# Performance work log

Hardware: AMD Instinct MI355X
Metric: run time of the kernel (lower is better)

Reference implementation:

```python
import jax, jax.numpy as jnp
import numpy as np

B, N_IN, N_OUT = 4096, 64, 64
M = N_IN * N_OUT


def setup_inputs() -> dict:
    key = jax.random.key(0)
    k1, k2, k3, k4 = jax.random.split(key, 4)
    I = jax.random.normal(k1, (B, N_IN, 4, 4), dtype=jnp.float32)
    # params: (rand - 0.5) * 1, matching torch init
    aW = (jax.random.uniform(k2, (M, 1, 1), dtype=jnp.float32) - 0.5)
    uW = (jax.random.uniform(k3, (M, 1, 3), dtype=jnp.float32) - 0.5)
    tW = (jax.random.uniform(k4, (M, 1, 3), dtype=jnp.float32) - 0.5)
    return {"I": I, "aW": aW, "uW": uW, "tW": tW}


def _build_WM(aW, uW, tW, n_in, n_out):
    m = aW.shape[0]
    a = aW.reshape(m, 1, 1)                       # angle per transform
    u = jax.nn.sigmoid(uW.reshape(m, 3))
    u = u / jnp.linalg.norm(u, axis=1, keepdims=True)  # unit axis
    ux, uy, uz = u[:, 0], u[:, 1], u[:, 2]
    z = jnp.zeros_like(ux)
    # skew-symmetric cross-product matrix K
    K = jnp.stack([z, -uz, uy,
                   uz, z, -ux,
                   -uy, ux, z], axis=1).reshape(m, 3, 3)
    uuT = u[:, :, None] * u[:, None, :]
    I3 = jnp.eye(3, dtype=aW.dtype)
    # Rodrigues: R = sin(a) K + cos(a)(I - uu^T) + uu^T
    rot = jnp.sin(a) * K + jnp.cos(a) * (I3 - uuT) + uuT
    top = jnp.concatenate([rot, tW.reshape(m, 3, 1)], axis=2)   # [m,3,4]
    bot = jnp.broadcast_to(jnp.array([[0.0, 0.0, 0.0, 1.0]], dtype=aW.dtype), (m, 1, 4))
    WM = jnp.concatenate([top, bot], axis=1)                    # [m,4,4]
    return WM.reshape(n_in, n_out, 4, 4)


def reference(I, aW, uW, tW):
    batch, n_in = I.shape[0], I.shape[1]
    n_out = aW.shape[0] // n_in
    WM = _build_WM(aW, uW, tW, n_in, n_out)       # [n_in, n_out, 4, 4] (batch-invariant)
    # A[b,j,k] = I[b,j] @ WM[j,k]
    A = jnp.einsum('bjxy,jkyz->jbkxz', I, WM)     # [n_in, B, n_out, 4, 4]
    init = jnp.broadcast_to(jnp.eye(4, dtype=I.dtype), (batch, n_out, 4, 4))
    def step(carry, Aj):
        return jnp.einsum('bkxy,bkyz->bkxz', carry, Aj), None
    O, _ = jax.lax.scan(step, init, A)            # sequential product over n_in
    return O                                      # [B, n_out, 4, 4]
```

## Files before the change

### kernel.cpp

```cpp
#include <hip/hip_runtime.h>

#define BATCH 4096
#define NIN   64
#define NOUT  64
#define M_TOT (NIN * NOUT)

__global__ __launch_bounds__(256) void build_wm_kernel(
    const float* __restrict__ aW, const float* __restrict__ uW,
    const float* __restrict__ tW, float4* __restrict__ WT) {
  int m = blockIdx.x * 256 + threadIdx.x;
  if (m >= M_TOT) return;
  int j = m >> 6, k = m & 63;

  float a  = aW[m];
  float ux = 1.f / (1.f + expf(-uW[3 * m + 0]));
  float uy = 1.f / (1.f + expf(-uW[3 * m + 1]));
  float uz = 1.f / (1.f + expf(-uW[3 * m + 2]));
  float inv = 1.f / sqrtf(ux * ux + uy * uy + uz * uz);
  ux *= inv; uy *= inv; uz *= inv;

  float sa = sinf(a), ca = cosf(a);
  float xx = ux * ux, yy = uy * uy, zz = uz * uz;
  float xy = ux * uy, xz = ux * uz, yz = uy * uz;

  float R00 = ca * (1.f - xx) + xx;
  float R01 = -sa * uz + ca * (-xy) + xy;
  float R02 =  sa * uy + ca * (-xz) + xz;
  float R10 =  sa * uz + ca * (-xy) + xy;
  float R11 = ca * (1.f - yy) + yy;
  float R12 = -sa * ux + ca * (-yz) + yz;
  float R20 = -sa * uy + ca * (-xz) + xz;
  float R21 =  sa * ux + ca * (-yz) + yz;
  float R22 = ca * (1.f - zz) + zz;

  float t0 = tW[3 * m + 0], t1 = tW[3 * m + 1], t2 = tW[3 * m + 2];

  WT[(j * 3 + 0) * 64 + k] = make_float4(R00, R01, R02, t0);
  WT[(j * 3 + 1) * 64 + k] = make_float4(R10, R11, R12, t1);
  WT[(j * 3 + 2) * 64 + k] = make_float4(R20, R21, R22, t2);
}


#define IMUL_TO(D0, D1, D2, D3, r, W0, W1, W2)                       \
  D0 = r.x * W0.x + r.y * W1.x + r.z * W2.x;                         \
  D1 = r.x * W0.y + r.y * W1.y + r.z * W2.y;                         \
  D2 = r.x * W0.z + r.y * W1.z + r.z * W2.z;                         \
  D3 = r.x * W0.w + r.y * W1.w + r.z * W2.w + r.w;

#define CMUL_ROW(x)                                                            \
  {                                                                            \
    float t0 = c[x*4+0]*A00 + c[x*4+1]*A10 + c[x*4+2]*A20 + c[x*4+3]*A30;      \
    float t1 = c[x*4+0]*A01 + c[x*4+1]*A11 + c[x*4+2]*A21 + c[x*4+3]*A31;      \
    float t2 = c[x*4+0]*A02 + c[x*4+1]*A12 + c[x*4+2]*A22 + c[x*4+3]*A32;      \
    float t3 = c[x*4+0]*A03 + c[x*4+1]*A13 + c[x*4+2]*A23 + c[x*4+3]*A33;      \
    c[x*4+0] = t0; c[x*4+1] = t1; c[x*4+2] = t2; c[x*4+3] = t3;                \
  }

#define STEP_FOLD(JJ, W0, W1, W2)                                              \
  {                                                                            \
    float4 r0 = Ib[(JJ) * 4 + 0], r1 = Ib[(JJ) * 4 + 1];                       \
    float4 r2 = Ib[(JJ) * 4 + 2], r3 = Ib[(JJ) * 4 + 3];                       \
    float A00, A01, A02, A03, A10, A11, A12, A13;                              \
    float A20, A21, A22, A23, A30, A31, A32, A33;                              \
    IMUL_TO(A00, A01, A02, A03, r0, W0, W1, W2)                                \
    IMUL_TO(A10, A11, A12, A13, r1, W0, W1, W2)                                \
    IMUL_TO(A20, A21, A22, A23, r2, W0, W1, W2)                                \
    IMUL_TO(A30, A31, A32, A33, r3, W0, W1, W2)                                \
    CMUL_ROW(0) CMUL_ROW(1) CMUL_ROW(2) CMUL_ROW(3)                            \
  }

__global__ __launch_bounds__(128) void chain_kernel(
    const float4* __restrict__ I4, const float4* __restrict__ WT,
    float4* __restrict__ O4) {
  const int lane = threadIdx.x & 63;
  const int half = threadIdx.x >> 6;
  const int b    = (int)blockIdx.x;

  const int ioff = __builtin_amdgcn_readfirstlane((b * NIN + half * 32) * 4);
  const float4* __restrict__ Ib = I4 + ioff;
  const float4* __restrict__ Wb = WT + (size_t)(half * 32 * 3) * 64 + lane;

  float c[16];
  float4 w0n, w1n, w2n;

  {
    float4 w0 = Wb[0], w1 = Wb[64], w2 = Wb[128];
    const float4* wp = Wb + 192;
    w0n = wp[0]; w1n = wp[64]; w2n = wp[128];

    float4 r0 = Ib[0], r1 = Ib[1], r2 = Ib[2], r3 = Ib[3];
    IMUL_TO(c[0],  c[1],  c[2],  c[3],  r0, w0, w1, w2)
    IMUL_TO(c[4],  c[5],  c[6],  c[7],  r1, w0, w1, w2)
    IMUL_TO(c[8],  c[9],  c[10], c[11], r2, w0, w1, w2)
    IMUL_TO(c[12], c[13], c[14], c[15], r3, w0, w1, w2)
  }

#pragma unroll 2
  for (int j = 1; j < 31; ++j) {
    float4 w0 = w0n, w1 = w1n, w2 = w2n;
    const float4* wp = Wb + (size_t)(j + 1) * 192;
    w0n = wp[0]; w1n = wp[64]; w2n = wp[128];
    STEP_FOLD(j, w0, w1, w2)
  }

  STEP_FOLD(31, w0n, w1n, w2n)

  __shared__ float P[64][17];
  if (half == 1) {
#pragma unroll
    for (int i = 0; i < 16; i++) P[lane][i] = c[i];
  }
  __syncthreads();
  if (half == 0) {
    float A00 = P[lane][0],  A01 = P[lane][1];
    float A02 = P[lane][2],  A03 = P[lane][3];
    float A10 = P[lane][4],  A11 = P[lane][5];
    float A12 = P[lane][6],  A13 = P[lane][7];
    float A20 = P[lane][8],  A21 = P[lane][9];
    float A22 = P[lane][10], A23 = P[lane][11];
    float A30 = P[lane][12], A31 = P[lane][13];
    float A32 = P[lane][14], A33 = P[lane][15];

    CMUL_ROW(0)
    CMUL_ROW(1)
    CMUL_ROW(2)
    CMUL_ROW(3)

    float4* o = O4 + ((size_t)b * NOUT + lane) * 4;
    o[0] = make_float4(c[0],  c[1],  c[2],  c[3]);
    o[1] = make_float4(c[4],  c[5],  c[6],  c[7]);
    o[2] = make_float4(c[8],  c[9],  c[10], c[11]);
    o[3] = make_float4(c[12], c[13], c[14], c[15]);
  }
}

extern "C" void kernel_launch(void* const* d_in, const int* in_sizes, int n_in,
                              void* d_out, int out_size, void* d_ws, size_t ws_size,
                              hipStream_t stream) {
  const float* I  = (const float*)d_in[0];
  const float* aW = (const float*)d_in[1];
  const float* uW = (const float*)d_in[2];
  const float* tW = (const float*)d_in[3];

  float4* WT = (float4*)d_ws;

  build_wm_kernel<<<M_TOT / 256, 256, 0, stream>>>(aW, uW, tW, WT);
  chain_kernel<<<BATCH, 128, 0, stream>>>((const float4*)I, WT, (float4*)d_out);
}
```

Baseline: 61.14 us.

## Process two batch elements per block to reuse loaded transform weights

Each block now handles two batch elements, so every W load from the workspace feeds two independent matrix chains. This halves global weight traffic per batch element and doubles the independent FMA work available per step for latency hiding. The explicit software prefetch of the next W is dropped in favour of unroll-by-4, and the grid is halved. The cost is higher register use, with two 16-float accumulators, and fewer blocks, which may reduce occupancy.

New measurement: 56.71 us. 1.08x faster.

```diff
diff --git a/kernel.cpp b/kernel.cpp
--- a/kernel.cpp
+++ b/kernel.cpp
@@ -47,26 +47,26 @@
   D2 = r.x * W0.z + r.y * W1.z + r.z * W2.z;                         \
   D3 = r.x * W0.w + r.y * W1.w + r.z * W2.w + r.w;
 
-#define CMUL_ROW(x)                                                            \
+#define CMUL_ROW_G(cc, x)                                                      \
   {                                                                            \
-    float t0 = c[x*4+0]*A00 + c[x*4+1]*A10 + c[x*4+2]*A20 + c[x*4+3]*A30;      \
-    float t1 = c[x*4+0]*A01 + c[x*4+1]*A11 + c[x*4+2]*A21 + c[x*4+3]*A31;      \
-    float t2 = c[x*4+0]*A02 + c[x*4+1]*A12 + c[x*4+2]*A22 + c[x*4+3]*A32;      \
-    float t3 = c[x*4+0]*A03 + c[x*4+1]*A13 + c[x*4+2]*A23 + c[x*4+3]*A33;      \
-    c[x*4+0] = t0; c[x*4+1] = t1; c[x*4+2] = t2; c[x*4+3] = t3;                \
+    float t0 = cc[x*4+0]*A00 + cc[x*4+1]*A10 + cc[x*4+2]*A20 + cc[x*4+3]*A30;  \
+    float t1 = cc[x*4+0]*A01 + cc[x*4+1]*A11 + cc[x*4+2]*A21 + cc[x*4+3]*A31;  \
+    float t2 = cc[x*4+0]*A02 + cc[x*4+1]*A12 + cc[x*4+2]*A22 + cc[x*4+3]*A32;  \
+    float t3 = cc[x*4+0]*A03 + cc[x*4+1]*A13 + cc[x*4+2]*A23 + cc[x*4+3]*A33;  \
+    cc[x*4+0] = t0; cc[x*4+1] = t1; cc[x*4+2] = t2; cc[x*4+3] = t3;            \
   }
 
-#define STEP_FOLD(JJ, W0, W1, W2)                                              \
+#define STEP_FOLD_G(cc, Ibase, JJ)                                             \
   {                                                                            \
-    float4 r0 = Ib[(JJ) * 4 + 0], r1 = Ib[(JJ) * 4 + 1];                       \
-    float4 r2 = Ib[(JJ) * 4 + 2], r3 = Ib[(JJ) * 4 + 3];                       \
+    float4 r0 = Ibase[(JJ) * 4 + 0], r1 = Ibase[(JJ) * 4 + 1];                 \
+    float4 r2 = Ibase[(JJ) * 4 + 2], r3 = Ibase[(JJ) * 4 + 3];                 \
     float A00, A01, A02, A03, A10, A11, A12, A13;                              \
     float A20, A21, A22, A23, A30, A31, A32, A33;                              \
-    IMUL_TO(A00, A01, A02, A03, r0, W0, W1, W2)                                \
-    IMUL_TO(A10, A11, A12, A13, r1, W0, W1, W2)                                \
-    IMUL_TO(A20, A21, A22, A23, r2, W0, W1, W2)                                \
-    IMUL_TO(A30, A31, A32, A33, r3, W0, W1, W2)                                \
-    CMUL_ROW(0) CMUL_ROW(1) CMUL_ROW(2) CMUL_ROW(3)                            \
+    IMUL_TO(A00, A01, A02, A03, r0, w0, w1, w2)                                \
+    IMUL_TO(A10, A11, A12, A13, r1, w0, w1, w2)                                \
+    IMUL_TO(A20, A21, A22, A23, r2, w0, w1, w2)                                \
+    IMUL_TO(A30, A31, A32, A33, r3, w0, w1, w2)                                \
+    CMUL_ROW_G(cc, 0) CMUL_ROW_G(cc, 1) CMUL_ROW_G(cc, 2) CMUL_ROW_G(cc, 3)   \
   }
 
 __global__ __launch_bounds__(128) void chain_kernel(
@@ -74,63 +74,77 @@
     float4* __restrict__ O4) {
   const int lane = threadIdx.x & 63;
   const int half = threadIdx.x >> 6;
-  const int b    = (int)blockIdx.x;
+  const int b0   = (int)blockIdx.x * 2;
 
-  const int ioff = __builtin_amdgcn_readfirstlane((b * NIN + half * 32) * 4);
-  const float4* __restrict__ Ib = I4 + ioff;
-  const float4* __restrict__ Wb = WT + (size_t)(half * 32 * 3) * 64 + lane;
+  const int ioff0 = __builtin_amdgcn_readfirstlane((b0 * NIN + half * 32) * 4);
+  const float4* __restrict__ Ib0 = I4 + ioff0;
+  const float4* __restrict__ Ib1 = Ib0 + NIN * 4;
+  const float4* __restrict__ Wb  = WT + (size_t)(half * 32 * 3) * 64 + lane;
 
-  float c[16];
-  float4 w0n, w1n, w2n;
+  float c0[16], c1[16];
 
   {
     float4 w0 = Wb[0], w1 = Wb[64], w2 = Wb[128];
-    const float4* wp = Wb + 192;
-    w0n = wp[0]; w1n = wp[64]; w2n = wp[128];
-
-    float4 r0 = Ib[0], r1 = Ib[1], r2 = Ib[2], r3 = Ib[3];
-    IMUL_TO(c[0],  c[1],  c[2],  c[3],  r0, w0, w1, w2)
-    IMUL_TO(c[4],  c[5],  c[6],  c[7],  r1, w0, w1, w2)
-    IMUL_TO(c[8],  c[9],  c[10], c[11], r2, w0, w1, w2)
-    IMUL_TO(c[12], c[13], c[14], c[15], r3, w0, w1, w2)
+    float4 r0 = Ib0[0], r1 = Ib0[1], r2 = Ib0[2], r3 = Ib0[3];
+    IMUL_TO(c0[0],  c0[1],  c0[2],  c0[3],  r0, w0, w1, w2)
+    IMUL_TO(c0[4],  c0[5],  c0[6],  c0[7],  r1, w0, w1, w2)
+    IMUL_TO(c0[8],  c0[9],  c0[10], c0[11], r2, w0, w1, w2)
+    IMUL_TO(c0[12], c0[13], c0[14], c0[15], r3, w0, w1, w2)
+    float4 s0 = Ib1[0], s1 = Ib1[1], s2 = Ib1[2], s3 = Ib1[3];
+    IMUL_TO(c1[0],  c1[1],  c1[2],  c1[3],  s0, w0, w1, w2)
+    IMUL_TO(c1[4],  c1[5],  c1[6],  c1[7],  s1, w0, w1, w2)
+    IMUL_TO(c1[8],  c1[9],  c1[10], c1[11], s2, w0, w1, w2)
+    IMUL_TO(c1[12], c1[13], c1[14], c1[15], s3, w0, w1, w2)
   }
 
-#pragma unroll 2
-  for (int j = 1; j < 31; ++j) {
-    float4 w0 = w0n, w1 = w1n, w2 = w2n;
-    const float4* wp = Wb + (size_t)(j + 1) * 192;
-    w0n = wp[0]; w1n = wp[64]; w2n = wp[128];
-    STEP_FOLD(j, w0, w1, w2)
+#pragma unroll 4
+  for (int j = 1; j < 32; ++j) {
+    float4 w0 = Wb[j * 192], w1 = Wb[j * 192 + 64], w2 = Wb[j * 192 + 128];
+    STEP_FOLD_G(c0, Ib0, j)
+    STEP_FOLD_G(c1, Ib1, j)
   }
 
-  STEP_FOLD(31, w0n, w1n, w2n)
-
-  __shared__ float P[64][17];
+  __shared__ float P[2][64][17];
   if (half == 1) {
 #pragma unroll
-    for (int i = 0; i < 16; i++) P[lane][i] = c[i];
+    for (int i = 0; i < 16; i++) P[0][lane][i] = c0[i];
+#pragma unroll
+    for (int i = 0; i < 16; i++) P[1][lane][i] = c1[i];
   }
   __syncthreads();
   if (half == 0) {
-    float A00 = P[lane][0],  A01 = P[lane][1];
-    float A02 = P[lane][2],  A03 = P[lane][3];
-    float A10 = P[lane][4],  A11 = P[lane][5];
-    float A12 = P[lane][6],  A13 = P[lane][7];
-    float A20 = P[lane][8],  A21 = P[lane][9];
-    float A22 = P[lane][10], A23 = P[lane][11];
-    float A30 = P[lane][12], A31 = P[lane][13];
-    float A32 = P[lane][14], A33 = P[lane][15];
-
-    CMUL_ROW(0)
-    CMUL_ROW(1)
-    CMUL_ROW(2)
-    CMUL_ROW(3)
-
-    float4* o = O4 + ((size_t)b * NOUT + lane) * 4;
-    o[0] = make_float4(c[0],  c[1],  c[2],  c[3]);
-    o[1] = make_float4(c[4],  c[5],  c[6],  c[7]);
-    o[2] = make_float4(c[8],  c[9],  c[10], c[11]);
-    o[3] = make_float4(c[12], c[13], c[14], c[15]);
+    {
+      float A00 = P[0][lane][0],  A01 = P[0][lane][1];
+      float A02 = P[0][lane][2],  A03 = P[0][lane][3];
+      float A10 = P[0][lane][4],  A11 = P[0][lane][5];
+      float A12 = P[0][lane][6],  A13 = P[0][lane][7];
+      float A20 = P[0][lane][8],  A21 = P[0][lane][9];
+      float A22 = P[0][lane][10], A23 = P[0][lane][11];
+      float A30 = P[0][lane][12], A31 = P[0][lane][13];
+      float A32 = P[0][lane][14], A33 = P[0][lane][15];
+      CMUL_ROW_G(c0, 0) CMUL_ROW_G(c0, 1) CMUL_ROW_G(c0, 2) CMUL_ROW_G(c0, 3)
+      float4* o = O4 + ((size_t)b0 * NOUT + lane) * 4;
+      o[0] = make_float4(c0[0],  c0[1],  c0[2],  c0[3]);
+      o[1] = make_float4(c0[4],  c0[5],  c0[6],  c0[7]);
+      o[2] = make_float4(c0[8],  c0[9],  c0[10], c0[11]);
+      o[3] = make_float4(c0[12], c0[13], c0[14], c0[15]);
+    }
+    {
+      float A00 = P[1][lane][0],  A01 = P[1][lane][1];
+      float A02 = P[1][lane][2],  A03 = P[1][lane][3];
+      float A10 = P[1][lane][4],  A11 = P[1][lane][5];
+      float A12 = P[1][lane][6],  A13 = P[1][lane][7];
+      float A20 = P[1][lane][8],  A21 = P[1][lane][9];
+      float A22 = P[1][lane][10], A23 = P[1][lane][11];
+      float A30 = P[1][lane][12], A31 = P[1][lane][13];
+      float A32 = P[1][lane][14], A33 = P[1][lane][15];
+      CMUL_ROW_G(c1, 0) CMUL_ROW_G(c1, 1) CMUL_ROW_G(c1, 2) CMUL_ROW_G(c1, 3)
+      float4* o = O4 + ((size_t)(b0 + 1) * NOUT + lane) * 4;
+      o[0] = make_float4(c1[0],  c1[1],  c1[2],  c1[3]);
+      o[1] = make_float4(c1[4],  c1[5],  c1[6],  c1[7]);
+      o[2] = make_float4(c1[8],  c1[9],  c1[10], c1[11]);
+      o[3] = make_float4(c1[12], c1[13], c1[14], c1[15]);
+    }
   }
 }
 
@@ -145,5 +159,5 @@
   float4* WT = (float4*)d_ws;
 
   build_wm_kernel<<<M_TOT / 256, 256, 0, stream>>>(aW, uW, tW, WT);
-  chain_kernel<<<BATCH, 128, 0, stream>>>((const float4*)I, WT, (float4*)d_out);
+  chain_kernel<<<BATCH / 2, 128, 0, stream>>>((const float4*)I, WT, (float4*)d_out);
 }
```

## Split chain product across four wavefronts per batch with LDS reduction

Applied to the files above, without the earlier changes.

Each block now uses four wavefronts, each multiplying a 16-step segment of the 64-matrix chain instead of two 32-step halves. Wavefront 0 then folds the other three partial products from shared memory in order. The explicit software prefetch of the next W rows is dropped in favour of direct loads under a larger unroll. The aim is to shorten the serial dependency chain per thread and raise latency hiding. The cost is more threads per block, a larger LDS buffer, and a longer serial fold at the end.

New measurement: 62.76 us. 2.7% more time.

```diff
diff --git a/kernel.cpp b/kernel.cpp
--- a/kernel.cpp
+++ b/kernel.cpp
@@ -56,38 +56,48 @@
     c[x*4+0] = t0; c[x*4+1] = t1; c[x*4+2] = t2; c[x*4+3] = t3;                \
   }
 
-#define STEP_FOLD(JJ, W0, W1, W2)                                              \
+#define STEP_FOLD(JJ)                                                          \
   {                                                                            \
+    float4 w0 = Wb[(JJ) * 192], w1 = Wb[(JJ) * 192 + 64],                      \
+           w2 = Wb[(JJ) * 192 + 128];                                          \
     float4 r0 = Ib[(JJ) * 4 + 0], r1 = Ib[(JJ) * 4 + 1];                       \
     float4 r2 = Ib[(JJ) * 4 + 2], r3 = Ib[(JJ) * 4 + 3];                       \
     float A00, A01, A02, A03, A10, A11, A12, A13;                              \
     float A20, A21, A22, A23, A30, A31, A32, A33;                              \
-    IMUL_TO(A00, A01, A02, A03, r0, W0, W1, W2)                                \
-    IMUL_TO(A10, A11, A12, A13, r1, W0, W1, W2)                                \
-    IMUL_TO(A20, A21, A22, A23, r2, W0, W1, W2)                                \
-    IMUL_TO(A30, A31, A32, A33, r3, W0, W1, W2)                                \
+    IMUL_TO(A00, A01, A02, A03, r0, w0, w1, w2)                                \
+    IMUL_TO(A10, A11, A12, A13, r1, w0, w1, w2)                                \
+    IMUL_TO(A20, A21, A22, A23, r2, w0, w1, w2)                                \
+    IMUL_TO(A30, A31, A32, A33, r3, w0, w1, w2)                                \
     CMUL_ROW(0) CMUL_ROW(1) CMUL_ROW(2) CMUL_ROW(3)                            \
   }
 
-__global__ __launch_bounds__(128) void chain_kernel(
+#define LDS_FOLD(q)                                                            \
+  {                                                                            \
+    float A00 = P[q][lane][0],  A01 = P[q][lane][1];                           \
+    float A02 = P[q][lane][2],  A03 = P[q][lane][3];                           \
+    float A10 = P[q][lane][4],  A11 = P[q][lane][5];                           \
+    float A12 = P[q][lane][6],  A13 = P[q][lane][7];                           \
+    float A20 = P[q][lane][8],  A21 = P[q][lane][9];                           \
+    float A22 = P[q][lane][10], A23 = P[q][lane][11];                          \
+    float A30 = P[q][lane][12], A31 = P[q][lane][13];                          \
+    float A32 = P[q][lane][14], A33 = P[q][lane][15];                          \
+    CMUL_ROW(0) CMUL_ROW(1) CMUL_ROW(2) CMUL_ROW(3)                            \
+  }
+
+__global__ __launch_bounds__(256) void chain_kernel(
     const float4* __restrict__ I4, const float4* __restrict__ WT,
     float4* __restrict__ O4) {
   const int lane = threadIdx.x & 63;
-  const int half = threadIdx.x >> 6;
+  const int wq   = threadIdx.x >> 6;
   const int b    = (int)blockIdx.x;
 
-  const int ioff = __builtin_amdgcn_readfirstlane((b * NIN + half * 32) * 4);
+  const int ioff = __builtin_amdgcn_readfirstlane((b * NIN + wq * 16) * 4);
   const float4* __restrict__ Ib = I4 + ioff;
-  const float4* __restrict__ Wb = WT + (size_t)(half * 32 * 3) * 64 + lane;
+  const float4* __restrict__ Wb = WT + (size_t)(wq * 16 * 3) * 64 + lane;
 
   float c[16];
-  float4 w0n, w1n, w2n;
-
   {
     float4 w0 = Wb[0], w1 = Wb[64], w2 = Wb[128];
-    const float4* wp = Wb + 192;
-    w0n = wp[0]; w1n = wp[64]; w2n = wp[128];
-
     float4 r0 = Ib[0], r1 = Ib[1], r2 = Ib[2], r3 = Ib[3];
     IMUL_TO(c[0],  c[1],  c[2],  c[3],  r0, w0, w1, w2)
     IMUL_TO(c[4],  c[5],  c[6],  c[7],  r1, w0, w1, w2)
@@ -95,36 +105,21 @@
     IMUL_TO(c[12], c[13], c[14], c[15], r3, w0, w1, w2)
   }
 
-#pragma unroll 2
-  for (int j = 1; j < 31; ++j) {
-    float4 w0 = w0n, w1 = w1n, w2 = w2n;
-    const float4* wp = Wb + (size_t)(j + 1) * 192;
-    w0n = wp[0]; w1n = wp[64]; w2n = wp[128];
-    STEP_FOLD(j, w0, w1, w2)
+#pragma unroll 5
+  for (int j = 1; j < 16; ++j) {
+    STEP_FOLD(j)
   }
 
-  STEP_FOLD(31, w0n, w1n, w2n)
-
-  __shared__ float P[64][17];
-  if (half == 1) {
+  __shared__ float P[4][64][17];
+  if (wq != 0) {
 #pragma unroll
-    for (int i = 0; i < 16; i++) P[lane][i] = c[i];
+    for (int i = 0; i < 16; i++) P[wq][lane][i] = c[i];
   }
   __syncthreads();
-  if (half == 0) {
-    float A00 = P[lane][0],  A01 = P[lane][1];
-    float A02 = P[lane][2],  A03 = P[lane][3];
-    float A10 = P[lane][4],  A11 = P[lane][5];
-    float A12 = P[lane][6],  A13 = P[lane][7];
-    float A20 = P[lane][8],  A21 = P[lane][9];
-    float A22 = P[lane][10], A23 = P[lane][11];
-    float A30 = P[lane][12], A31 = P[lane][13];
-    float A32 = P[lane][14], A33 = P[lane][15];
-
-    CMUL_ROW(0)
-    CMUL_ROW(1)
-    CMUL_ROW(2)
-    CMUL_ROW(3)
+  if (wq == 0) {
+    LDS_FOLD(1)
+    LDS_FOLD(2)
+    LDS_FOLD(3)
 
     float4* o = O4 + ((size_t)b * NOUT + lane) * 4;
     o[0] = make_float4(c[0],  c[1],  c[2],  c[3]);
@@ -145,5 +140,5 @@
   float4* WT = (float4*)d_ws;
 
   build_wm_kernel<<<M_TOT / 256, 256, 0, stream>>>(aW, uW, tW, WT);
-  chain_kernel<<<BATCH, 128, 0, stream>>>((const float4*)I, WT, (float4*)d_out);
+  chain_kernel<<<BATCH, 256, 0, stream>>>((const float4*)I, WT, (float4*)d_out);
 }
```
